# Kernel tuning notes

Measured on AMD Instinct MI355X. Metric: run time of the kernel, lower is better.

The kernel has to match this reference:

```python
import jax, jax.numpy as jnp
import numpy as np

TEMPERATURE = 0.5


def _cos_sim_flat(a, b):
    # row-normalize then full similarity matrix, flattened (matches torch.mm(a_n, b_n.T).flatten())
    a_n = a / jnp.linalg.norm(a, axis=1, keepdims=True)
    b_n = b / jnp.linalg.norm(b, axis=1, keepdims=True)
    return (a_n @ b_n.T).reshape(-1)


def setup_inputs() -> dict:
    key = jax.random.key(0)
    k1, k2, k3 = jax.random.split(key, 3)
    N, D = 4096, 2048
    return {
        "x_source": jax.random.normal(k1, (N, D), dtype=jnp.float32),
        "x_bc_target": jax.random.normal(k2, (N, D), dtype=jnp.float32),
        "x_raw_target": jax.random.normal(k3, (N, D), dtype=jnp.float32),
    }


def reference(x_source, x_bc_target, x_raw_target):
    sim_pos = _cos_sim_flat(x_source, x_bc_target)  # [N*N]
    sim_neg = _cos_sim_flat(x_source, x_raw_target)  # [N*N]
    # denom = sum_j exp(sim_neg_j / T); loss_i = -log(exp(sim_pos_i/T)/denom)
    # = -sim_pos_i/T + logsumexp(sim_neg/T); mean over i. Same math as the
    # original scalar loops, computed as one fused reduction.
    log_denom = jax.nn.logsumexp(sim_neg / TEMPERATURE)
    cl_loss = jnp.mean(log_denom - sim_pos / TEMPERATURE)
    return cl_loss
```

## Files before the change

kernel.cpp:

```cpp
#include <hip/hip_runtime.h>

#define NR 4096
#define DD 2048
#define INV_T 2.0f
#define QS4 64.0f
#define ACC4_TO_LOGIT (INV_T / (QS4 * QS4))

typedef __attribute__((ext_vector_type(2))) float floatx2;
typedef __attribute__((ext_vector_type(4))) float floatx4;
typedef __attribute__((ext_vector_type(4))) int int4v;
typedef __attribute__((ext_vector_type(8))) int int8v;

static __device__ __forceinline__ void async_copy16(const void* g, void* lds) {
  __builtin_amdgcn_global_load_lds((const __attribute__((address_space(1))) void*)g,
                                   (__attribute__((address_space(3))) void*)lds,
                                   16, 0, 0);
}

static __device__ __forceinline__ unsigned int enc4(float x) {
  float u = fminf(fabsf(x), 6.0f);
  int c = (u >= 0.25f) + (u >= 0.75f) + (u >= 1.25f) + (u >= 1.75f) +
          (u >= 2.5f) + (u >= 3.5f) + (u >= 5.0f);
  return (unsigned)(c | (x < 0.f ? 8 : 0));
}

static __device__ __forceinline__ unsigned int pack8_fp4(
    const float4& v0, const float4& v1, float s) {
  return enc4(v0.x * s)        | (enc4(v0.y * s) << 4)  |
         (enc4(v0.z * s) << 8) | (enc4(v0.w * s) << 12) |
         (enc4(v1.x * s) << 16)| (enc4(v1.y * s) << 20) |
         (enc4(v1.z * s) << 24)| (enc4(v1.w * s) << 28);
}

__global__ __launch_bounds__(256) void zero_kernel(floatx4* z) {
  #pragma unroll
  for (int i = 0; i < 4; i++)
    z[threadIdx.x + 256 * i] = floatx4{0.f, 0.f, 0.f, 0.f};
}

__global__ __launch_bounds__(256) void normalize_colsum_kernel(
    const float* __restrict__ src, const float* __restrict__ bc,
    const float* __restrict__ raw,
    unsigned int* __restrict__ a4, unsigned int* __restrict__ c4,
    float* __restrict__ s_a, float* __restrict__ s_b) {
  const int mat = blockIdx.y;
  const int tid = threadIdx.x;
  const int lane = tid & 63;
  const int wave = tid >> 6;
  const float* base = (mat == 0) ? src : ((mat == 1) ? bc : raw);
  unsigned int* q4 = (mat == 0) ? a4 : c4;

  float acc[32];
  #pragma unroll
  for (int i = 0; i < 32; i++) acc[i] = 0.f;

  #pragma unroll
  for (int r = 0; r < 4; r++) {
    const int row = blockIdx.x * 16 + wave * 4 + r;
    const float4* rp = (const float4*)(base + (size_t)row * DD);
    float4 v[8];
    #pragma unroll
    for (int c = 0; c < 4; c++) {
      v[2 * c]     = rp[lane * 2 + 128 * c];
      v[2 * c + 1] = rp[lane * 2 + 1 + 128 * c];
    }
    float ss = 0.f;
    #pragma unroll
    for (int c = 0; c < 8; c++)
      ss += v[c].x * v[c].x + v[c].y * v[c].y + v[c].z * v[c].z + v[c].w * v[c].w;
    #pragma unroll
    for (int off = 1; off < 64; off <<= 1) ss += __shfl_xor(ss, off, 64);
    const float sinv = rsqrtf(ss);

    if (mat != 2) {
      #pragma unroll
      for (int c = 0; c < 8; c++) {
        acc[c * 4 + 0] += v[c].x * sinv; acc[c * 4 + 1] += v[c].y * sinv;
        acc[c * 4 + 2] += v[c].z * sinv; acc[c * 4 + 3] += v[c].w * sinv;
      }
    }
    if (mat != 1) {
      const float s4 = sinv * QS4;
      #pragma unroll
      for (int c = 0; c < 4; c++)
        q4[row * 256 + lane + 64 * c] = pack8_fp4(v[2 * c], v[2 * c + 1], s4);
    }
  }
  if (mat == 2) return;

  __shared__ float lsum[4][2048];
  #pragma unroll
  for (int c = 0; c < 4; c++) {
    *(floatx4*)&lsum[wave][8 * lane + 512 * c] =
        floatx4{acc[8 * c], acc[8 * c + 1], acc[8 * c + 2], acc[8 * c + 3]};
    *(floatx4*)&lsum[wave][8 * lane + 512 * c + 4] =
        floatx4{acc[8 * c + 4], acc[8 * c + 5], acc[8 * c + 6], acc[8 * c + 7]};
  }
  __syncthreads();
  float* dst = (mat == 0) ? s_a : s_b;
  #pragma unroll
  for (int k = 0; k < 8; k++) {
    const int col = tid + 256 * k;
    atomicAdd(&dst[col],
              lsum[0][col] + lsum[1][col] + lsum[2][col] + lsum[3][col]);
  }
}

__global__ __launch_bounds__(256, 2) void gemm_expsum_kernel(
    const unsigned char* __restrict__ a4, const unsigned char* __restrict__ c4,
    float* __restrict__ S_part) {
  __shared__ unsigned char As[2][128 * 128];
  __shared__ unsigned char Cs[2][128 * 128];
  const int tid = threadIdx.x;
  const int lane = tid & 63;
  const int wave = tid >> 6;
  const int wr = wave >> 1;
  const int wc = wave & 1;
  const int quad = lane >> 4;
  const int l16 = lane & 15;

  const int lin = blockIdx.y * 32 + blockIdx.x;
  const int xcd = lin & 7;
  const int idx = lin >> 3;
  const int br = (xcd >> 1) * 8 + (idx >> 4);
  const int bc = (xcd & 1) * 16 + (idx & 15);

  floatx4 acc[4][4] = {};

  const int wrow = lane >> 3;
  const int csrc = (lane & 7) ^ (wrow & 7);
  const unsigned char* gA[4];
  const unsigned char* gC[4];
  int ldsOff[4];
  #pragma unroll
  for (int q = 0; q < 4; q++) {
    const int m = wave * 4 + q;
    const int row = m * 8 + wrow;
    gA[q] = a4 + (size_t)(br * 128 + row) * 1024 + csrc * 16;
    gC[q] = c4 + (size_t)(bc * 128 + row) * 1024 + csrc * 16;
    ldsOff[q] = m * 1024;
  }

  #pragma unroll
  for (int q = 0; q < 4; q++) {
    async_copy16(gA[q], &As[0][ldsOff[q]]);
    async_copy16(gC[q], &Cs[0][ldsOff[q]]);
    gA[q] += 128; gC[q] += 128;
  }

  const int NKT = DD / 256;
  #pragma unroll 2
  for (int kt = 0; kt < NKT; kt++) {
    const int cur = kt & 1;
    __syncthreads();

    if (kt < NKT - 1) {
      #pragma unroll
      for (int q = 0; q < 4; q++) {
        async_copy16(gA[q], &As[cur ^ 1][ldsOff[q]]);
        async_copy16(gC[q], &Cs[cur ^ 1][ldsOff[q]]);
        gA[q] += 128; gC[q] += 128;
      }
    }

    int4v af[2][4], bf[2][4];
    #pragma unroll
    for (int s = 0; s < 2; s++) {
      #pragma unroll
      for (int i = 0; i < 4; i++) {
        const int r = wr * 64 + i * 16 + l16;
        const int pc = (s * 4 + quad) ^ (r & 7);
        af[s][i] = *(const int4v*)&As[cur][r * 128 + pc * 16];
      }
      #pragma unroll
      for (int j = 0; j < 4; j++) {
        const int r = wc * 64 + j * 16 + l16;
        const int pc = (s * 4 + quad) ^ (r & 7);
        bf[s][j] = *(const int4v*)&Cs[cur][r * 128 + pc * 16];
      }
    }
    #pragma unroll
    for (int s = 0; s < 2; s++)
      #pragma unroll
      for (int i = 0; i < 4; i++) {
        const int8v a8v = int8v{af[s][i][0], af[s][i][1], af[s][i][2],
                                af[s][i][3], 0, 0, 0, 0};
        #pragma unroll
        for (int j = 0; j < 4; j++) {
          const int8v b8v = int8v{bf[s][j][0], bf[s][j][1], bf[s][j][2],
                                  bf[s][j][3], 0, 0, 0, 0};
          acc[i][j] = __builtin_amdgcn_mfma_scale_f32_16x16x128_f8f6f4(
              a8v, b8v, acc[i][j], 4 , 4 ,
              0, 0x7F7F7F7F, 0, 0x7F7F7F7F );
        }
      }
  }

  float local = 0.f;
  #pragma unroll
  for (int i = 0; i < 4; i++)
    #pragma unroll
    for (int j = 0; j < 4; j++)
      #pragma unroll
      for (int r = 0; r < 4; r++)
        local += __expf(acc[i][j][r] * ACC4_TO_LOGIT);
  #pragma unroll
  for (int off = 32; off > 0; off >>= 1) local += __shfl_down(local, off, 64);
  __shared__ float red[4];
  if (lane == 0) red[wave] = local;
  __syncthreads();
  if (tid == 0) S_part[br * 32 + bc] = red[0] + red[1] + red[2] + red[3];
}

__global__ __launch_bounds__(256) void finalize_kernel(
    const float* __restrict__ s_a, const float* __restrict__ s_b,
    const float* __restrict__ S_part, float* __restrict__ out) {
  const int tid = threadIdx.x;
  float dot = 0.f, se = 0.f;
  #pragma unroll
  for (int k = 0; k < 8; k++)
    dot += s_a[tid + 256 * k] * s_b[tid + 256 * k];
  #pragma unroll
  for (int k = 0; k < 4; k++) se += S_part[tid + 256 * k];
  #pragma unroll
  for (int off = 32; off > 0; off >>= 1) {
    dot += __shfl_down(dot, off, 64);
    se  += __shfl_down(se, off, 64);
  }
  __shared__ float redd[4], reds[4];
  if ((tid & 63) == 0) { redd[tid >> 6] = dot; reds[tid >> 6] = se; }
  __syncthreads();
  if (tid == 0) {
    const float dt = redd[0] + redd[1] + redd[2] + redd[3];
    const float st = reds[0] + reds[1] + reds[2] + reds[3];
    out[0] = logf(st) - dt * (INV_T / ((float)NR * (float)NR));
  }
}

extern "C" void kernel_launch(void* const* d_in, const int* in_sizes, int n_in,
                              void* d_out, int out_size, void* d_ws, size_t ws_size,
                              hipStream_t stream) {
  const float* src = (const float*)d_in[0];
  const float* bc  = (const float*)d_in[1];
  const float* raw = (const float*)d_in[2];

  char* ws = (char*)d_ws;
  unsigned int* a4 = (unsigned int*)ws;
  unsigned int* c4 = (unsigned int*)(ws + (size_t)4 * 1024 * 1024);
  float* zb  = (float*)(ws + (size_t)8 * 1024 * 1024);
  float* s_a = zb;
  float* s_b = zb + DD;
  float* S_part = (float*)(ws + (size_t)8 * 1024 * 1024 + 32 * 1024);

  zero_kernel<<<1, 256, 0, stream>>>((floatx4*)zb);
  normalize_colsum_kernel<<<dim3(NR / 16, 3), 256, 0, stream>>>(
      src, bc, raw, a4, c4, s_a, s_b);
  gemm_expsum_kernel<<<dim3(32, 32), 256, 0, stream>>>(
      (const unsigned char*)a4, (const unsigned char*)c4, S_part);
  finalize_kernel<<<1, 256, 0, stream>>>(s_a, s_b, S_part, (float*)d_out);
}
```

Before: 149.4 us.

## Switch GEMM to 32x32x64 scaled MFMA and fold finalize into last block

The FP4 GEMM inner loop now issues 32x32x64 scaled MFMAs into a 2x2 grid of 16-wide accumulators per wave, in place of the 4x4 grid of 16x16x128 MFMAs. This cuts the instruction count and changes the LDS fragment load pattern. The separate finalize kernel is removed: each block publishes its partial sum, and the last block to arrive, tracked by an atomic float counter, computes the final loss. This saves a kernel launch but adds a threadfence and atomic overhead to every block.

```diff
diff --git a/kernel.cpp b/kernel.cpp
--- a/kernel.cpp
+++ b/kernel.cpp
@@ -8,6 +8,7 @@
 
 typedef __attribute__((ext_vector_type(2))) float floatx2;
 typedef __attribute__((ext_vector_type(4))) float floatx4;
+typedef __attribute__((ext_vector_type(16))) float floatx16;
 typedef __attribute__((ext_vector_type(4))) int int4v;
 typedef __attribute__((ext_vector_type(8))) int int8v;
 
@@ -32,10 +33,11 @@
          (enc4(v1.z * s) << 24)| (enc4(v1.w * s) << 28);
 }
 
-__global__ __launch_bounds__(256) void zero_kernel(floatx4* z) {
+__global__ __launch_bounds__(256) void zero_kernel(float* z) {
   #pragma unroll
   for (int i = 0; i < 4; i++)
-    z[threadIdx.x + 256 * i] = floatx4{0.f, 0.f, 0.f, 0.f};
+    *(floatx4*)&z[4 * (threadIdx.x + 256 * i)] = floatx4{0.f, 0.f, 0.f, 0.f};
+  if (threadIdx.x == 0) z[4096] = 0.f;
 }
 
 __global__ __launch_bounds__(256) void normalize_colsum_kernel(
@@ -108,7 +110,9 @@
 
 __global__ __launch_bounds__(256, 2) void gemm_expsum_kernel(
     const unsigned char* __restrict__ a4, const unsigned char* __restrict__ c4,
-    float* __restrict__ S_part) {
+    float* __restrict__ S_part, float* __restrict__ counter,
+    const float* __restrict__ s_a, const float* __restrict__ s_b,
+    float* __restrict__ out) {
   __shared__ unsigned char As[2][128 * 128];
   __shared__ unsigned char Cs[2][128 * 128];
   const int tid = threadIdx.x;
@@ -116,8 +120,8 @@
   const int wave = tid >> 6;
   const int wr = wave >> 1;
   const int wc = wave & 1;
-  const int quad = lane >> 4;
-  const int l16 = lane & 15;
+  const int half = lane >> 5;
+  const int l32 = lane & 31;
 
   const int lin = blockIdx.y * 32 + blockIdx.x;
   const int xcd = lin & 7;
@@ -125,7 +129,7 @@
   const int br = (xcd >> 1) * 8 + (idx >> 4);
   const int bc = (xcd & 1) * 16 + (idx & 15);
 
-  floatx4 acc[4][4] = {};
+  floatx16 acc[2][2] = {};
 
   const int wrow = lane >> 3;
   const int csrc = (lane & 7) ^ (wrow & 7);
@@ -163,33 +167,33 @@
       }
     }
 
-    int4v af[2][4], bf[2][4];
-    #pragma unroll
-    for (int s = 0; s < 2; s++) {
-      #pragma unroll
-      for (int i = 0; i < 4; i++) {
-        const int r = wr * 64 + i * 16 + l16;
-        const int pc = (s * 4 + quad) ^ (r & 7);
+    int4v af[4][2], bf[4][2];
+    #pragma unroll
+    for (int s = 0; s < 4; s++) {
+      #pragma unroll
+      for (int i = 0; i < 2; i++) {
+        const int r = wr * 64 + i * 32 + l32;
+        const int pc = (s * 2 + half) ^ (r & 7);
         af[s][i] = *(const int4v*)&As[cur][r * 128 + pc * 16];
       }
       #pragma unroll
-      for (int j = 0; j < 4; j++) {
-        const int r = wc * 64 + j * 16 + l16;
-        const int pc = (s * 4 + quad) ^ (r & 7);
+      for (int j = 0; j < 2; j++) {
+        const int r = wc * 64 + j * 32 + l32;
+        const int pc = (s * 2 + half) ^ (r & 7);
         bf[s][j] = *(const int4v*)&Cs[cur][r * 128 + pc * 16];
       }
     }
     #pragma unroll
-    for (int s = 0; s < 2; s++)
-      #pragma unroll
-      for (int i = 0; i < 4; i++) {
+    for (int s = 0; s < 4; s++)
+      #pragma unroll
+      for (int i = 0; i < 2; i++) {
         const int8v a8v = int8v{af[s][i][0], af[s][i][1], af[s][i][2],
                                 af[s][i][3], 0, 0, 0, 0};
         #pragma unroll
-        for (int j = 0; j < 4; j++) {
+        for (int j = 0; j < 2; j++) {
           const int8v b8v = int8v{bf[s][j][0], bf[s][j][1], bf[s][j][2],
                                   bf[s][j][3], 0, 0, 0, 0};
-          acc[i][j] = __builtin_amdgcn_mfma_scale_f32_16x16x128_f8f6f4(
+          acc[i][j] = __builtin_amdgcn_mfma_scale_f32_32x32x64_f8f6f4(
               a8v, b8v, acc[i][j], 4 , 4 ,
               0, 0x7F7F7F7F, 0, 0x7F7F7F7F );
         }
@@ -198,30 +202,35 @@
 
   float local = 0.f;
   #pragma unroll
-  for (int i = 0; i < 4; i++)
-    #pragma unroll
-    for (int j = 0; j < 4; j++)
-      #pragma unroll
-      for (int r = 0; r < 4; r++)
+  for (int i = 0; i < 2; i++)
+    #pragma unroll
+    for (int j = 0; j < 2; j++)
+      #pragma unroll
+      for (int r = 0; r < 16; r++)
         local += __expf(acc[i][j][r] * ACC4_TO_LOGIT);
   #pragma unroll
   for (int off = 32; off > 0; off >>= 1) local += __shfl_down(local, off, 64);
   __shared__ float red[4];
   if (lane == 0) red[wave] = local;
   __syncthreads();
-  if (tid == 0) S_part[br * 32 + bc] = red[0] + red[1] + red[2] + red[3];
-}
-
-__global__ __launch_bounds__(256) void finalize_kernel(
-    const float* __restrict__ s_a, const float* __restrict__ s_b,
-    const float* __restrict__ S_part, float* __restrict__ out) {
-  const int tid = threadIdx.x;
+  if (tid == 0)
+    atomicExch(&S_part[br * 32 + bc], red[0] + red[1] + red[2] + red[3]);
+
+  __threadfence();
+  __syncthreads();
+  __shared__ bool amLast;
+  if (tid == 0) amLast = (atomicAdd(counter, 1.0f) == 1023.0f);
+  __syncthreads();
+  if (!amLast) return;
+  __threadfence();
+
   float dot = 0.f, se = 0.f;
   #pragma unroll
   for (int k = 0; k < 8; k++)
     dot += s_a[tid + 256 * k] * s_b[tid + 256 * k];
   #pragma unroll
-  for (int k = 0; k < 4; k++) se += S_part[tid + 256 * k];
+  for (int k = 0; k < 4; k++)
+    se += atomicAdd(&S_part[tid + 256 * k], 0.f);
   #pragma unroll
   for (int off = 32; off > 0; off >>= 1) {
     dot += __shfl_down(dot, off, 64);
@@ -250,12 +259,13 @@
   float* zb  = (float*)(ws + (size_t)8 * 1024 * 1024);
   float* s_a = zb;
   float* s_b = zb + DD;
+  float* counter = zb + 2 * DD;
   float* S_part = (float*)(ws + (size_t)8 * 1024 * 1024 + 32 * 1024);
 
-  zero_kernel<<<1, 256, 0, stream>>>((floatx4*)zb);
+  zero_kernel<<<1, 256, 0, stream>>>(zb);
   normalize_colsum_kernel<<<dim3(NR / 16, 3), 256, 0, stream>>>(
       src, bc, raw, a4, c4, s_a, s_b);
   gemm_expsum_kernel<<<dim3(32, 32), 256, 0, stream>>>(
-      (const unsigned char*)a4, (const unsigned char*)c4, S_part);
-  finalize_kernel<<<1, 256, 0, stream>>>(s_a, s_b, S_part, (float*)d_out);
-}
+      (const unsigned char*)a4, (const unsigned char*)c4, S_part, counter,
+      s_a, s_b, (float*)d_out);
+}
```

New measurement: 205.5 us. +37.6%, slower.
